# Performance work log

Measured on AMD Instinct MI355X. Metric: run time of the kernel, lower is better.

Reference implementation:

```python
import jax, jax.numpy as jnp
import numpy as np

N, D, HID = 16384, 1024, 4096
IN_DIM = 4 * D + 1
LN_EPS = 1e-5


def setup_inputs() -> dict:
    key = jax.random.key(0)
    ks = jax.random.split(key, 8)
    # xavier_uniform for bilinear: bound = sqrt(6/(d+d))
    bb = float(np.sqrt(6.0 / (D + D)))
    w1b = float(np.sqrt(1.0 / IN_DIM))  # torch Linear default init bound
    w2b = float(np.sqrt(1.0 / HID))
    return {
        "zA": jax.random.normal(ks[0], (N, D), dtype=jnp.float32),
        "zB": jax.random.normal(ks[1], (N, D), dtype=jnp.float32),
        "bilinear": jax.random.uniform(ks[2], (D, D), minval=-bb, maxval=bb, dtype=jnp.float32),
        "ln_g": jnp.ones((IN_DIM,), dtype=jnp.float32),
        "ln_b": jnp.zeros((IN_DIM,), dtype=jnp.float32),
        "W1": jax.random.uniform(ks[3], (IN_DIM, HID), minval=-w1b, maxval=w1b, dtype=jnp.float32),
        "b1": jax.random.uniform(ks[4], (HID,), minval=-w1b, maxval=w1b, dtype=jnp.float32),
        "W2": jax.random.uniform(ks[5], (HID, D), minval=-w2b, maxval=w2b, dtype=jnp.float32),
        "b2": jax.random.uniform(ks[6], (D,), minval=-w2b, maxval=w2b, dtype=jnp.float32),
    }


def reference(zA, zB, bilinear, ln_g, ln_b, W1, b1, W2, b2):
    had = zA * zB                                   # [N, D]
    diff = jnp.abs(zA - zB)                         # [N, D]
    # diag(zA @ W @ zB^T) == sum((zA @ W) * zB, -1)  -- O(N d^2) not O(N^2 d)
    s = jnp.sum((zA @ bilinear) * zB, axis=-1, keepdims=True)  # [N, 1]
    x = jnp.concatenate([zA, zB, had, diff, s], axis=1)        # [N, 4D+1]
    # LayerNorm over last dim
    mu = jnp.mean(x, axis=-1, keepdims=True)
    var = jnp.mean(jnp.square(x - mu), axis=-1, keepdims=True)
    x = (x - mu) * jax.lax.rsqrt(var + LN_EPS) * ln_g + ln_b
    # Linear -> GELU (exact/erf, torch default) -> Linear -> GELU; dropout off (eval)
    h = jax.nn.gelu(x @ W1 + b1, approximate=False)            # [N, HID]
    out = jax.nn.gelu(h @ W2 + b2, approximate=False)          # [N, D]
    return out
```

## Files before the change

### kernel.cpp

```cpp
#include <hip/hip_runtime.h>
#include <math.h>

#define NROWS 16384
#define DDIM  1024
#define HIDD  4096

typedef __bf16 bf16;
typedef bf16 bf16x8 __attribute__((ext_vector_type(8)));
typedef bf16 bf16x4 __attribute__((ext_vector_type(4)));
typedef float f32x4 __attribute__((ext_vector_type(4)));

__device__ __forceinline__ float gelu_erf(float x) {
  return 0.5f * x * (1.0f + erff(x * 0.70710678118654752f));
}

__device__ __forceinline__ void gld16(const bf16* g, bf16* l) {
  __builtin_amdgcn_global_load_lds(
      (const __attribute__((address_space(1))) void*)g,
      (__attribute__((address_space(3))) void*)l, 16, 0, 0);
}

__global__ __launch_bounds__(256) void cast_bf16_k(const float* __restrict__ in,
                                                   bf16* __restrict__ out) {
  size_t i = (size_t)blockIdx.x * blockDim.x + threadIdx.x;
  float4 v = ((const float4*)in)[i];
  bf16x4 o = {(bf16)v.x, (bf16)v.y, (bf16)v.z, (bf16)v.w};
  ((bf16x4*)out)[i] = o;
}

__global__ __launch_bounds__(256) void transpose_cast_k(const float* __restrict__ in,
                                                        bf16* __restrict__ out,
                                                        int R, int C) {
  __shared__ float tile[32][33];
  int bx = blockIdx.x * 32, by = blockIdx.y * 32;
  int tx = threadIdx.x, ty = threadIdx.y;
  #pragma unroll
  for (int i = ty; i < 32; i += 8)
    tile[i][tx] = in[(size_t)(by + i) * C + bx + tx];
  __syncthreads();
  #pragma unroll
  for (int i = ty; i < 32; i += 8)
    out[(size_t)(bx + i) * R + by + tx] = (bf16)tile[tx][i];
}

__global__ __launch_bounds__(256) void rowfuse_k(
    const float* __restrict__ zA, const float* __restrict__ zB,
    const bf16* __restrict__ t, const float* __restrict__ lng,
    const float* __restrict__ lnb, bf16* __restrict__ x,
    float* __restrict__ s_ln) {
  int row = blockIdx.x, tid = threadIdx.x;
  float4 a4 = ((const float4*)(zA + (size_t)row * DDIM))[tid];
  float4 b4 = ((const float4*)(zB + (size_t)row * DDIM))[tid];
  bf16x4 t4 = ((const bf16x4*)(t + (size_t)row * DDIM))[tid];
  float av[4] = {a4.x, a4.y, a4.z, a4.w};
  float bv[4] = {b4.x, b4.y, b4.z, b4.w};
  float hv[4], dv[4];
  float s1 = 0.f, s2 = 0.f, sd = 0.f;
  #pragma unroll
  for (int j = 0; j < 4; j++) {
    hv[j] = av[j] * bv[j];
    dv[j] = fabsf(av[j] - bv[j]);
    s1 += av[j] + bv[j] + hv[j] + dv[j];
    s2 += av[j]*av[j] + bv[j]*bv[j] + hv[j]*hv[j] + dv[j]*dv[j];
    sd += (float)t4[j] * bv[j];
  }
  #pragma unroll
  for (int off = 32; off > 0; off >>= 1) {
    s1 += __shfl_xor(s1, off, 64);
    s2 += __shfl_xor(s2, off, 64);
    sd += __shfl_xor(sd, off, 64);
  }
  __shared__ float red[3][4];
  int wave = tid >> 6;
  if ((tid & 63) == 0) { red[0][wave] = s1; red[1][wave] = s2; red[2][wave] = sd; }
  __syncthreads();
  s1 = red[0][0] + red[0][1] + red[0][2] + red[0][3];
  s2 = red[1][0] + red[1][1] + red[1][2] + red[1][3];
  float s = red[2][0] + red[2][1] + red[2][2] + red[2][3];
  const float inv = 1.0f / 4097.0f;
  float mu = (s1 + s) * inv;
  float var = (s2 + s * s) * inv - mu * mu;
  float rs = rsqrtf(var + 1e-5f);
  bf16* xr = x + (size_t)row * 4096;
  #define WRITE_SEG(si, vals)                                            \
  {                                                                      \
    float4 gg = ((const float4*)lng)[(si)*256 + tid];                    \
    float4 bb = ((const float4*)lnb)[(si)*256 + tid];                    \
    const float* gp = (const float*)&gg;                                 \
    const float* bp = (const float*)&bb;                                 \
    bf16x4 o;                                                            \
    _Pragma("unroll") for (int j = 0; j < 4; j++)                        \
        o[j] = (bf16)((vals[j] - mu) * rs * gp[j] + bp[j]);              \
    ((bf16x4*)xr)[(si)*256 + tid] = o;                                   \
  }
  WRITE_SEG(0, av)
  WRITE_SEG(1, bv)
  WRITE_SEG(2, hv)
  WRITE_SEG(3, dv)
  #undef WRITE_SEG
  if (tid == 0) s_ln[row] = (s - mu) * rs * lng[4096] + lnb[4096];
}

template <int EPI>
__global__ __launch_bounds__(256) void gemm_bt_k(
    const bf16* __restrict__ A, const bf16* __restrict__ B, int K, int Nout,
    void* __restrict__ Cout, const float* __restrict__ bias,
    const float* __restrict__ srow, const float* __restrict__ wlast) {
  __shared__ alignas(16) bf16 As[128 * 64];
  __shared__ alignas(16) bf16 Bs[128 * 64];
  const int tid = threadIdx.x;
  const int wave = tid >> 6, lane = tid & 63;
  const int wm = wave >> 1, wn = wave & 1;
  const int lrow = lane & 15, quad = lane >> 4;
  const size_t rowA0 = (size_t)blockIdx.y * 128;
  const size_t rowB0 = (size_t)blockIdx.x * 128;

  f32x4 acc[4][4] = {};

  const int lchunk = (tid & 7) ^ ((tid >> 3) & 7);
  const bf16* gA = A + (rowA0 + (tid >> 3)) * (size_t)K + lchunk * 8;
  const bf16* gB = B + (rowB0 + (tid >> 3)) * (size_t)K + lchunk * 8;

  for (int kb = 0; kb < K; kb += 64) {
    const bf16* pa = gA + kb;
    const bf16* pb = gB + kb;
    #pragma unroll
    for (int it = 0; it < 4; it++) {
      gld16(pa + (size_t)it * 32 * K, As + it * 2048 + wave * 512);
      gld16(pb + (size_t)it * 32 * K, Bs + it * 2048 + wave * 512);
    }
    __syncthreads();
    #pragma unroll
    for (int kk = 0; kk < 2; kk++) {
      const int cla = ((kk * 4 + quad) ^ (lrow & 7)) * 8;
      bf16x8 af[4], bfr[4];
      #pragma unroll
      for (int mi = 0; mi < 4; mi++)
        af[mi] = *(const bf16x8*)(As + (wm * 64 + mi * 16 + lrow) * 64 + cla);
      #pragma unroll
      for (int ni = 0; ni < 4; ni++)
        bfr[ni] = *(const bf16x8*)(Bs + (wn * 64 + ni * 16 + lrow) * 64 + cla);
      #pragma unroll
      for (int mi = 0; mi < 4; mi++)
        #pragma unroll
        for (int ni = 0; ni < 4; ni++)
          acc[mi][ni] = __builtin_amdgcn_mfma_f32_16x16x32_bf16(af[mi], bfr[ni], acc[mi][ni], 0, 0, 0);
    }
    __syncthreads();
  }

  const size_t ldc = (size_t)Nout;
  #pragma unroll
  for (int mi = 0; mi < 4; mi++) {
    size_t row = rowA0 + wm * 64 + mi * 16 + quad * 4;
    float srv[4];
    if (EPI == 1) {
      #pragma unroll
      for (int r = 0; r < 4; r++) srv[r] = srow[row + r];
    }
    #pragma unroll
    for (int ni = 0; ni < 4; ni++) {
      size_t col = rowB0 + wn * 64 + ni * 16 + lrow;
      float bvv = (EPI != 0) ? bias[col] : 0.0f;
      float wl = (EPI == 1) ? wlast[col] : 0.0f;
      #pragma unroll
      for (int r = 0; r < 4; r++) {
        float v = acc[mi][ni][r];
        if (EPI == 1) v += bvv + srv[r] * wl;
        if (EPI == 2) v += bvv;
        if (EPI != 0) v = gelu_erf(v);
        size_t idx = (row + r) * ldc + col;
        if (EPI == 2) ((float*)Cout)[idx] = v;
        else ((bf16*)Cout)[idx] = (bf16)v;
      }
    }
  }
}

#define CFENCE asm volatile("" ::: "memory")
__global__ __launch_bounds__(512, 2) void gemm256_epi1_k(
    const bf16* __restrict__ A, const bf16* __restrict__ B, int K, int Nout,
    bf16* __restrict__ Cout, const float* __restrict__ bias,
    const float* __restrict__ srow, const float* __restrict__ wlast) {
  __shared__ alignas(16) bf16 As[2][2][8192];
  __shared__ alignas(16) bf16 Bs[2][2][8192];
  const int tid = threadIdx.x;
  const int wave = tid >> 6, lane = tid & 63;
  const int wm = wave >> 2, wn = wave & 3;
  const int lrow = lane & 15, quad = lane >> 4;
  const int cswz = ((quad ^ ((lrow >> 1) & 3)) << 3);

  const int id = blockIdx.x;
  const int nrow = gridDim.x >> 4;
  int bxt, byt;
  if ((nrow & 15) == 0) {
    const int xcd = id & 7, k = id >> 3;
    const int rect = k >> 5, pos = k & 31;
    byt = rect * 16 + ((xcd >> 1) << 2) + (pos >> 3);
    bxt = ((xcd & 1) << 3) + (pos & 7);
  } else {
    bxt = id & 15;
    byt = id >> 4;
  }
  const size_t rowA0 = (size_t)byt * 256;
  const size_t rowB0 = (size_t)bxt * 256;
  const int Kmask = K - 1;

  const int sr = tid >> 2;
  const int sq = (tid & 3) ^ ((sr >> 1) & 3);
  const bf16* gA = A + (rowA0 + sr) * (size_t)K + sq * 8;
  const bf16* gB = B + (rowB0 + sr) * (size_t)K + sq * 8;
  const size_t rstep = 128 * (size_t)K;
  const int wofs = wave * 512;

  f32x4 acc[8][4] = {};

#define STG_A(b, h, ko) { const bf16* s_ = gA + ((ko) & Kmask);          \
    gld16(s_, &As[b][h][wofs]); gld16(s_ + rstep, &As[b][h][4096 + wofs]); }
#define STG_B(b, h, ko) { const bf16* s_ = gB + ((ko) & Kmask);          \
    gld16(s_, &Bs[b][h][wofs]); gld16(s_ + rstep, &Bs[b][h][4096 + wofs]); }

  STG_A(0, 0, 0)  STG_B(0, 0, 0)
  STG_A(0, 1, 32) STG_B(0, 1, 32)
  STG_A(1, 0, 64) STG_B(1, 0, 64)
  asm volatile("s_waitcnt vmcnt(4)" ::: "memory");
  __builtin_amdgcn_s_barrier();
  CFENCE;

  bf16x8 af[8], bfr[2];
  const int arow = wm * 128 + lrow;
  const int brow = wn * 64 + lrow;

#define LD_A(b, h) { _Pragma("unroll") for (int mi = 0; mi < 8; mi++)    \
    af[mi] = *(const bf16x8*)(&As[b][h][(arow + mi * 16) * 32 + cswz]); }
#define LD_B(b, h, nlo) { _Pragma("unroll") for (int nj = 0; nj < 2; nj++) \
    bfr[nj] = *(const bf16x8*)(&Bs[b][h][(brow + ((nlo) + nj) * 16) * 32 + cswz]); }
#define MFMA_HALF(nlo) { _Pragma("unroll") for (int mi = 0; mi < 8; mi++) {           \
    acc[mi][nlo] = __builtin_amdgcn_mfma_f32_16x16x32_bf16(af[mi], bfr[0], acc[mi][nlo], 0, 0, 0);       \
    acc[mi][(nlo)+1] = __builtin_amdgcn_mfma_f32_16x16x32_bf16(af[mi], bfr[1], acc[mi][(nlo)+1], 0, 0, 0); } }
#define PH(bufc, khc, nlo, LOADA, STAGE, VW) {                           \
    LD_B(bufc, khc, nlo)                                                 \
    if (LOADA) LD_A(bufc, khc)                                           \
    STAGE                                                                \
    CFENCE;                                                              \
    __builtin_amdgcn_s_barrier();                                        \
    CFENCE;                                                              \
    __builtin_amdgcn_s_setprio(1);                                       \
    MFMA_HALF(nlo)                                                       \
    __builtin_amdgcn_s_setprio(0);                                       \
    CFENCE;                                                              \
    VW                                                                   \
    __builtin_amdgcn_s_barrier();                                        \
    CFENCE; }

  const int NI = K >> 7;
  int kb = 0;
  #pragma unroll 1
  for (int i = 0; i < NI; ++i, kb += 128) {
    PH(0, 0, 0, 1, STG_A(1, 1, kb + 96), )
    PH(0, 0, 2, 0, STG_B(1, 1, kb + 96), )
    PH(0, 1, 0, 1, STG_A(0, 0, kb + 128), )
    PH(0, 1, 2, 0, STG_B(0, 0, kb + 128),
       asm volatile("s_waitcnt vmcnt(4)" ::: "memory");)
    PH(1, 0, 0, 1, STG_A(0, 1, kb + 160), )
    PH(1, 0, 2, 0, STG_B(0, 1, kb + 160), )
    PH(1, 1, 0, 1, STG_A(1, 0, kb + 192), )
    PH(1, 1, 2, 0, STG_B(1, 0, kb + 192),
       asm volatile("s_waitcnt vmcnt(4)" ::: "memory");)
  }
  asm volatile("s_waitcnt vmcnt(0)" ::: "memory");
#undef PH
#undef MFMA_HALF
#undef LD_B
#undef LD_A
#undef STG_B
#undef STG_A

  const size_t ldc = (size_t)Nout;
  #pragma unroll
  for (int mi = 0; mi < 8; mi++) {
    size_t row = rowA0 + wm * 128 + mi * 16 + quad * 4;
    float srv[4];
    #pragma unroll
    for (int r = 0; r < 4; r++) srv[r] = srow[row + r];
    #pragma unroll
    for (int ni = 0; ni < 4; ni++) {
      size_t col = rowB0 + wn * 64 + ni * 16 + lrow;
      float bvv = bias[col];
      float wl = wlast[col];
      #pragma unroll
      for (int r = 0; r < 4; r++) {
        float v = acc[mi][ni][r] + bvv + srv[r] * wl;
        v = gelu_erf(v);
        Cout[(row + r) * ldc + col] = (bf16)v;
      }
    }
  }
}

extern "C" void kernel_launch(void* const* d_in, const int* in_sizes, int n_in,
                              void* d_out, int out_size, void* d_ws, size_t ws_size,
                              hipStream_t stream) {
  const float* zA  = (const float*)d_in[0];
  const float* zB  = (const float*)d_in[1];
  const float* bil = (const float*)d_in[2];
  const float* lng = (const float*)d_in[3];
  const float* lnb = (const float*)d_in[4];
  const float* W1  = (const float*)d_in[5];
  const float* b1  = (const float*)d_in[6];
  const float* W2  = (const float*)d_in[7];
  const float* b2  = (const float*)d_in[8];
  float* out = (float*)d_out;

  char* ws = (char*)d_ws;
  const size_t SZ_BILT = (size_t)DDIM * DDIM * 2;
  const size_t SZ_W1T  = (size_t)4096 * 4096 * 2;
  const size_t SZ_W2T  = (size_t)DDIM * HIDD * 2;
  const size_t PERSIST = SZ_BILT + SZ_W1T + SZ_W2T;

  int C = 0;
  for (int cand = NROWS; cand >= 512; cand >>= 1) {
    size_t need = PERSIST + (size_t)16384 * cand + (size_t)4 * cand + 1024;
    if (need <= ws_size) { C = cand; break; }
  }
  if (C == 0) return;

  bf16* bilT = (bf16*)ws;
  bf16* W1T  = (bf16*)(ws + SZ_BILT);
  bf16* W2T  = (bf16*)(ws + SZ_BILT + SZ_W1T);
  char* dyn  = ws + PERSIST;
  bf16*  r1    = (bf16*)dyn;
  bf16*  zA_bf = r1;
  bf16*  t_bf  = r1 + (size_t)C * 1024;
  bf16*  h_bf  = r1;
  bf16*  x_bf  = (bf16*)(dyn + (size_t)8192 * C);
  float* s_ln  = (float*)(dyn + (size_t)16384 * C);

  dim3 tb(32, 8);
  transpose_cast_k<<<dim3(DDIM / 32, DDIM / 32), tb, 0, stream>>>(bil, bilT, DDIM, DDIM);
  transpose_cast_k<<<dim3(HIDD / 32, 4096 / 32), tb, 0, stream>>>(W1, W1T, 4096, HIDD);
  transpose_cast_k<<<dim3(DDIM / 32, HIDD / 32), tb, 0, stream>>>(W2, W2T, HIDD, DDIM);

  for (int r0 = 0; r0 < NROWS; r0 += C) {
    const float* zAc = zA + (size_t)r0 * DDIM;
    const float* zBc = zB + (size_t)r0 * DDIM;

    cast_bf16_k<<<(C * DDIM / 4) / 256, 256, 0, stream>>>(zAc, zA_bf);

    gemm_bt_k<0><<<dim3(DDIM / 128, C / 128), 256, 0, stream>>>(
        zA_bf, bilT, DDIM, DDIM, t_bf, nullptr, nullptr, nullptr);

    rowfuse_k<<<C, 256, 0, stream>>>(zAc, zBc, t_bf, lng, lnb, x_bf, s_ln);

    gemm256_epi1_k<<<dim3((HIDD / 256) * (C / 256)), 512, 0, stream>>>(
        x_bf, W1T, 4096, HIDD, h_bf, b1, s_ln, W1 + (size_t)4096 * HIDD);

    gemm_bt_k<2><<<dim3(DDIM / 128, C / 128), 256, 0, stream>>>(
        h_bf, W2T, 4096, DDIM, out + (size_t)r0 * DDIM, b2, nullptr, nullptr);
  }
}
```

Before: 1.085 ms.

## Retile W1 GEMM to 256x128 blocks with 3-stage LDS ring pipeline

Replaces the 256x256, 512-thread W1 GEMM kernel with a 256x128, 256-thread kernel. Shared-memory staging changes from a double-buffered half-K scheme to a three-slot ring of 32-wide K tiles, with a new vmcnt wait pattern. The XCD-aware block-to-tile remapping is updated for the new grid shape. The intent is more blocks for better CU occupancy and load balance, at the cost of lower arithmetic intensity per block and more B reloads. The loop trip count is hardcoded for K=4096 (42 iterations plus a 2-tile tail).

```diff
diff --git a/kernel.cpp b/kernel.cpp
--- a/kernel.cpp
+++ b/kernel.cpp
@@ -178,103 +178,111 @@
 }
 
 #define CFENCE asm volatile("" ::: "memory")
-__global__ __launch_bounds__(512, 2) void gemm256_epi1_k(
+__global__ __launch_bounds__(256, 2) void gemm256x128_epi1_k(
     const bf16* __restrict__ A, const bf16* __restrict__ B, int K, int Nout,
     bf16* __restrict__ Cout, const float* __restrict__ bias,
     const float* __restrict__ srow, const float* __restrict__ wlast) {
-  __shared__ alignas(16) bf16 As[2][2][8192];
-  __shared__ alignas(16) bf16 Bs[2][2][8192];
+  __shared__ alignas(16) bf16 As[3][8192];
+  __shared__ alignas(16) bf16 Bs[3][4096];
   const int tid = threadIdx.x;
   const int wave = tid >> 6, lane = tid & 63;
-  const int wm = wave >> 2, wn = wave & 3;
+  const int wm = wave >> 1, wn = wave & 1;
   const int lrow = lane & 15, quad = lane >> 4;
   const int cswz = ((quad ^ ((lrow >> 1) & 3)) << 3);
 
   const int id = blockIdx.x;
-  const int nrow = gridDim.x >> 4;
+  const int ncol = Nout >> 7;
+  const int nrow = (int)(gridDim.x / ncol);
   int bxt, byt;
-  if ((nrow & 15) == 0) {
+  if (ncol == 32 && nrow == 32) {
     const int xcd = id & 7, k = id >> 3;
-    const int rect = k >> 5, pos = k & 31;
-    byt = rect * 16 + ((xcd >> 1) << 2) + (pos >> 3);
-    bxt = ((xcd & 1) << 3) + (pos & 7);
+    const int rect = k >> 6, pos = k & 63;
+    byt = ((xcd >> 1) << 3) + (pos >> 3);
+    bxt = ((xcd & 1) << 4) + (rect << 3) + (pos & 7);
   } else {
-    bxt = id & 15;
-    byt = id >> 4;
+    bxt = id % ncol;
+    byt = id / ncol;
   }
   const size_t rowA0 = (size_t)byt * 256;
-  const size_t rowB0 = (size_t)bxt * 256;
+  const size_t rowB0 = (size_t)bxt * 128;
   const int Kmask = K - 1;
-
-  const int sr = tid >> 2;
-  const int sq = (tid & 3) ^ ((sr >> 1) & 3);
-  const bf16* gA = A + (rowA0 + sr) * (size_t)K + sq * 8;
-  const bf16* gB = B + (rowB0 + sr) * (size_t)K + sq * 8;
-  const size_t rstep = 128 * (size_t)K;
+  const size_t Ksz = (size_t)K;
+
+  const int sq = (tid & 3) ^ ((tid >> 3) & 3);
+  const bf16* gA = A + (rowA0 + (tid >> 2)) * Ksz + sq * 8;
+  const bf16* gB = B + (rowB0 + (tid >> 2)) * Ksz + sq * 8;
   const int wofs = wave * 512;
 
   f32x4 acc[8][4] = {};
 
-#define STG_A(b, h, ko) { const bf16* s_ = gA + ((ko) & Kmask);          \
-    gld16(s_, &As[b][h][wofs]); gld16(s_ + rstep, &As[b][h][4096 + wofs]); }
-#define STG_B(b, h, ko) { const bf16* s_ = gB + ((ko) & Kmask);          \
-    gld16(s_, &Bs[b][h][wofs]); gld16(s_ + rstep, &Bs[b][h][4096 + wofs]); }
-
-  STG_A(0, 0, 0)  STG_B(0, 0, 0)
-  STG_A(0, 1, 32) STG_B(0, 1, 32)
-  STG_A(1, 0, 64) STG_B(1, 0, 64)
-  asm volatile("s_waitcnt vmcnt(4)" ::: "memory");
-  __builtin_amdgcn_s_barrier();
-  CFENCE;
+#define STG_A3(rb, ko) { const bf16* s_ = gA + ((ko) & Kmask);           \
+    gld16(s_,             &As[rb][0 * 2048 + wofs]);                     \
+    gld16(s_ +  64 * Ksz, &As[rb][1 * 2048 + wofs]);                     \
+    gld16(s_ + 128 * Ksz, &As[rb][2 * 2048 + wofs]);                     \
+    gld16(s_ + 192 * Ksz, &As[rb][3 * 2048 + wofs]); }
+#define STG_B3(rb, ko) { const bf16* s_ = gB + ((ko) & Kmask);           \
+    gld16(s_,             &Bs[rb][0 * 2048 + wofs]);                     \
+    gld16(s_ +  64 * Ksz, &Bs[rb][1 * 2048 + wofs]); }
 
   bf16x8 af[8], bfr[2];
   const int arow = wm * 128 + lrow;
   const int brow = wn * 64 + lrow;
 
-#define LD_A(b, h) { _Pragma("unroll") for (int mi = 0; mi < 8; mi++)    \
-    af[mi] = *(const bf16x8*)(&As[b][h][(arow + mi * 16) * 32 + cswz]); }
-#define LD_B(b, h, nlo) { _Pragma("unroll") for (int nj = 0; nj < 2; nj++) \
-    bfr[nj] = *(const bf16x8*)(&Bs[b][h][(brow + ((nlo) + nj) * 16) * 32 + cswz]); }
+#define LD_A3(rb) { _Pragma("unroll") for (int mi = 0; mi < 8; mi++)     \
+    af[mi] = *(const bf16x8*)(&As[rb][(arow + mi * 16) * 32 + cswz]); }
+#define LD_B3(rb, nlo) { _Pragma("unroll") for (int nj = 0; nj < 2; nj++) \
+    bfr[nj] = *(const bf16x8*)(&Bs[rb][(brow + ((nlo) + nj) * 16) * 32 + cswz]); }
 #define MFMA_HALF(nlo) { _Pragma("unroll") for (int mi = 0; mi < 8; mi++) {           \
     acc[mi][nlo] = __builtin_amdgcn_mfma_f32_16x16x32_bf16(af[mi], bfr[0], acc[mi][nlo], 0, 0, 0);       \
     acc[mi][(nlo)+1] = __builtin_amdgcn_mfma_f32_16x16x32_bf16(af[mi], bfr[1], acc[mi][(nlo)+1], 0, 0, 0); } }
-#define PH(bufc, khc, nlo, LOADA, STAGE, VW) {                           \
-    LD_B(bufc, khc, nlo)                                                 \
-    if (LOADA) LD_A(bufc, khc)                                           \
-    STAGE                                                                \
+#define TILE(rb, rs, ko) {                                               \
+    LD_B3(rb, 0)                                                         \
+    LD_A3(rb)                                                            \
+    STG_A3(rs, ko)                                                       \
     CFENCE;                                                              \
     __builtin_amdgcn_s_barrier();                                        \
     CFENCE;                                                              \
     __builtin_amdgcn_s_setprio(1);                                       \
-    MFMA_HALF(nlo)                                                       \
+    MFMA_HALF(0)                                                         \
     __builtin_amdgcn_s_setprio(0);                                       \
     CFENCE;                                                              \
-    VW                                                                   \
+    __builtin_amdgcn_s_barrier();                                        \
+    CFENCE;                                                              \
+    LD_B3(rb, 2)                                                         \
+    STG_B3(rs, ko)                                                       \
+    asm volatile("s_waitcnt vmcnt(6)" ::: "memory");                     \
+    CFENCE;                                                              \
+    __builtin_amdgcn_s_barrier();                                        \
+    CFENCE;                                                              \
+    __builtin_amdgcn_s_setprio(1);                                       \
+    MFMA_HALF(2)                                                         \
+    __builtin_amdgcn_s_setprio(0);                                       \
+    CFENCE;                                                              \
     __builtin_amdgcn_s_barrier();                                        \
     CFENCE; }
 
-  const int NI = K >> 7;
-  int kb = 0;
+  STG_A3(0, 0)  STG_B3(0, 0)
+  STG_A3(1, 32) STG_B3(1, 32)
+  asm volatile("s_waitcnt vmcnt(6)" ::: "memory");
+  __builtin_amdgcn_s_barrier();
+  CFENCE;
+
+  int kb = 64;
   #pragma unroll 1
-  for (int i = 0; i < NI; ++i, kb += 128) {
-    PH(0, 0, 0, 1, STG_A(1, 1, kb + 96), )
-    PH(0, 0, 2, 0, STG_B(1, 1, kb + 96), )
-    PH(0, 1, 0, 1, STG_A(0, 0, kb + 128), )
-    PH(0, 1, 2, 0, STG_B(0, 0, kb + 128),
-       asm volatile("s_waitcnt vmcnt(4)" ::: "memory");)
-    PH(1, 0, 0, 1, STG_A(0, 1, kb + 160), )
-    PH(1, 0, 2, 0, STG_B(0, 1, kb + 160), )
-    PH(1, 1, 0, 1, STG_A(1, 0, kb + 192), )
-    PH(1, 1, 2, 0, STG_B(1, 0, kb + 192),
-       asm volatile("s_waitcnt vmcnt(4)" ::: "memory");)
-  }
+  for (int i = 0; i < 42; ++i, kb += 96) {
+    TILE(0, 2, kb)
+    TILE(1, 0, kb + 32)
+    TILE(2, 1, kb + 64)
+  }
+  TILE(0, 2, kb)
+  TILE(1, 0, kb + 32)
   asm volatile("s_waitcnt vmcnt(0)" ::: "memory");
-#undef PH
+#undef TILE
 #undef MFMA_HALF
-#undef LD_B
-#undef LD_A
-#undef STG_B
-#undef STG_A
+#undef LD_B3
+#undef LD_A3
+#undef STG_B3
+#undef STG_A3
 
   const size_t ldc = (size_t)Nout;
   #pragma unroll
@@ -352,7 +360,7 @@
 
     rowfuse_k<<<C, 256, 0, stream>>>(zAc, zBc, t_bf, lng, lnb, x_bf, s_ln);
 
-    gemm256_epi1_k<<<dim3((HIDD / 256) * (C / 256)), 512, 0, stream>>>(
+    gemm256x128_epi1_k<<<dim3((HIDD / 128) * (C / 256)), 256, 0, stream>>>(
         x_bf, W1T, 4096, HIDD, h_bf, b1, s_ln, W1 + (size_t)4096 * HIDD);
 
     gemm_bt_k<2><<<dim3(DDIM / 128, C / 128), 256, 0, stream>>>(
```

New measurement: 1.054 ms. 1.03x faster.
